# Optimization experiments

Measured on AMD Instinct MI355X. Metric: run time of the kernel, lower is better.

Reference implementation:

```python
import jax, jax.numpy as jnp
import numpy as np
from jax import lax


def setup_inputs() -> dict:
    key = jax.random.key(0)
    k1, k2 = jax.random.split(key)
    L, B, d = 2048, 16, 1024
    x = jax.random.normal(k1, (L, B, d), dtype=jnp.float32)
    val_range = (3.0 / d) ** 0.5
    weight = jax.random.uniform(k2, (d, 3 * d), dtype=jnp.float32,
                                minval=-val_range, maxval=val_range)
    bias = jnp.zeros((2 * d,), dtype=jnp.float32)
    c0 = jnp.zeros((B, d), dtype=jnp.float32)
    return {"x": x, "weight": weight, "bias": bias, "c0": c0}


def reference(x, weight, bias, c0):
    # x: [L, B, d]; weight: [d, 3d]; bias: [2d]; c0: [B, d]
    L, B, d = x.shape
    u = (x.reshape(-1, d) @ weight).reshape(L, B, d, 3)
    x_tilde = u[..., 0]                               # [L, B, d]
    forget = jax.nn.sigmoid(u[..., 1] + bias[:d])     # [L, B, d]
    reset = jax.nn.sigmoid(u[..., 2] + bias[d:])      # [L, B, d]
    # k == 3 case: x_prime is the raw input (highway connection)
    x_prime = x

    def step(c_prev, ft_xt):
        ft, xt = ft_xt
        c = (c_prev - xt) * ft + xt
        return c, c

    c_last, cs = lax.scan(step, c0, (forget, x_tilde))
    g = jnp.tanh(cs)  # activation_type == 1
    h = (g - x_prime) * reset + x_prime
    return h, c_last
```

## Files before the change

kernel.cpp:

```cpp
#include <hip/hip_runtime.h>

#define L_SEQ 2048
#define BATCH 16
#define DDIM  1024
#define MDIM  (L_SEQ * BATCH)
#define NDIM  (3 * DDIM)
#define KDIM  DDIM
#define CH    (BATCH * DDIM)
#define NSEG  32
#define SEGL  64

typedef __attribute__((ext_vector_type(8))) short short8;
typedef __attribute__((ext_vector_type(4))) float f32x4;

static __device__ __forceinline__ unsigned short f2bf(float f) {
  unsigned int u = __builtin_bit_cast(unsigned int, f);
  unsigned int lsb = (u >> 16) & 1u;
  u += 0x7fffu + lsb;
  return (unsigned short)(u >> 16);
}
static __device__ __forceinline__ float bf2f(unsigned short s) {
  unsigned int u = ((unsigned int)s) << 16;
  return __builtin_bit_cast(float, u);
}

static __device__ __forceinline__ void gll16(const void* g, void* l) {
  __builtin_amdgcn_global_load_lds(
      (const __attribute__((address_space(1))) unsigned int*)g,
      (__attribute__((address_space(3))) unsigned int*)l, 16, 0, 0);
}


__global__ void k_convert_x(const float4* __restrict__ x, ushort4* __restrict__ xb, int n4) {
  int i = blockIdx.x * blockDim.x + threadIdx.x;
  int stride = gridDim.x * blockDim.x;
  for (; i < n4; i += stride) {
    float4 v = x[i];
    ushort4 o;
    o.x = f2bf(v.x); o.y = f2bf(v.y); o.z = f2bf(v.z); o.w = f2bf(v.w);
    xb[i] = o;
  }
}

__global__ void k_convert_w(const float* __restrict__ w, unsigned short* __restrict__ wb) {
  int gid = blockIdx.x * 256 + threadIdx.x;
  int k = gid & (KDIM - 1);
  int n = gid >> 10;
  int col = (n < DDIM) ? 3 * n : (n < 2 * DDIM) ? 3 * (n - DDIM) + 1 : 3 * (n - 2 * DDIM) + 2;
  wb[gid] = f2bf(w[(size_t)k * NDIM + col]);
}


#define MFMA1(I, J, A, B) \
  acc[I][J] = __builtin_amdgcn_mfma_f32_16x16x32_bf16(A, B, acc[I][J], 0, 0, 0);

#define MFMAQ(BASE, A0, A1, A2, A3, B0, B1, B2, B3)      \
  MFMA1(BASE + 0, 0, A0, B0) MFMA1(BASE + 0, 1, A0, B1)  \
  MFMA1(BASE + 0, 2, A0, B2) MFMA1(BASE + 0, 3, A0, B3)  \
  MFMA1(BASE + 1, 0, A1, B0) MFMA1(BASE + 1, 1, A1, B1)  \
  MFMA1(BASE + 1, 2, A1, B2) MFMA1(BASE + 1, 3, A1, B3)  \
  MFMA1(BASE + 2, 0, A2, B0) MFMA1(BASE + 2, 1, A2, B1)  \
  MFMA1(BASE + 2, 2, A2, B2) MFMA1(BASE + 2, 3, A2, B3)  \
  MFMA1(BASE + 3, 0, A3, B0) MFMA1(BASE + 3, 1, A3, B1)  \
  MFMA1(BASE + 3, 2, A3, B2) MFMA1(BASE + 3, 3, A3, B3)

#define TILE64(T) do {                                                        \
  const char* bufC = LDSc + ((T) & 1) * 65536;                                \
  char*       bufN = LDSc + (((T) + 1) & 1) * 65536;                          \
  const int stA = (((T) + 1) & 15) * 128;                                     \
         \
  gll16(srcA0 + stA, bufN + dstOff);                                          \
  gll16(srcA1 + stA, bufN + 8192 + dstOff);                                   \
  gll16(srcB0 + stA, bufN + 32768 + dstOff);                                  \
  gll16(srcB1 + stA, bufN + 40960 + dstOff);                                  \
  gll16(srcA0 + stA + 64, bufN + 16384 + dstOff);                             \
  gll16(srcA1 + stA + 64, bufN + 24576 + dstOff);                             \
  gll16(srcB0 + stA + 64, bufN + 49152 + dstOff);                             \
  gll16(srcB1 + stA + 64, bufN + 57344 + dstOff);                             \
  __builtin_amdgcn_sched_barrier(0);                                          \
      \
  a0 = *(const short8*)(bufC + aRd);                                          \
  a1 = *(const short8*)(bufC + aRd + 1024);                                   \
  a2 = *(const short8*)(bufC + aRd + 2048);                                   \
  a3 = *(const short8*)(bufC + aRd + 3072);                                   \
  b0 = *(const short8*)(bufC + 32768 + bRd);                                  \
  b1 = *(const short8*)(bufC + 32768 + bRd + 1024);                           \
  b2 = *(const short8*)(bufC + 32768 + bRd + 2048);                           \
  b3 = *(const short8*)(bufC + 32768 + bRd + 3072);                           \
  na0 = *(const short8*)(bufC + aRd + 4096);                                  \
  na1 = *(const short8*)(bufC + aRd + 5120);                                  \
  na2 = *(const short8*)(bufC + aRd + 6144);                                  \
  na3 = *(const short8*)(bufC + aRd + 7168);                                  \
  __builtin_amdgcn_s_setprio(1);                                              \
  MFMAQ(0, a0, a1, a2, a3, b0, b1, b2, b3)                                    \
  __builtin_amdgcn_s_setprio(0);                                              \
  a0 = *(const short8*)(bufC + 16384 + aRd);                                  \
  a1 = *(const short8*)(bufC + 16384 + aRd + 1024);                           \
  a2 = *(const short8*)(bufC + 16384 + aRd + 2048);                           \
  a3 = *(const short8*)(bufC + 16384 + aRd + 3072);                           \
  nb0 = *(const short8*)(bufC + 49152 + bRd);                                 \
  nb1 = *(const short8*)(bufC + 49152 + bRd + 1024);                          \
  nb2 = *(const short8*)(bufC + 49152 + bRd + 2048);                          \
  nb3 = *(const short8*)(bufC + 49152 + bRd + 3072);                          \
  __builtin_amdgcn_s_setprio(1);                                              \
  MFMAQ(4, na0, na1, na2, na3, b0, b1, b2, b3)                                \
  __builtin_amdgcn_s_setprio(0);                                              \
  na0 = *(const short8*)(bufC + 16384 + aRd + 4096);                          \
  na1 = *(const short8*)(bufC + 16384 + aRd + 5120);                          \
  na2 = *(const short8*)(bufC + 16384 + aRd + 6144);                          \
  na3 = *(const short8*)(bufC + 16384 + aRd + 7168);                          \
  __builtin_amdgcn_s_setprio(1);                                              \
  MFMAQ(0, a0, a1, a2, a3, nb0, nb1, nb2, nb3)                                \
  MFMAQ(4, na0, na1, na2, na3, nb0, nb1, nb2, nb3)                            \
  __builtin_amdgcn_s_setprio(0);                                              \
          \
  asm volatile("s_waitcnt vmcnt(0)" ::: "memory");                            \
  __builtin_amdgcn_s_barrier();                                               \
} while (0)

__global__ __launch_bounds__(512, 2) void k_gemm256(
    const unsigned short* __restrict__ xb,
    const unsigned short* __restrict__ wb,
    const float* __restrict__ bias,
    unsigned short* __restrict__ xtb,
    unsigned short* __restrict__ fbuf,
    unsigned short* __restrict__ rbuf) {
  __shared__ char LDS[131072];
  char* LDSc = LDS;

  const int tid  = threadIdx.x;
  const int lane = tid & 63;
  const int wid  = tid >> 6;
  const int wr   = wid >> 2;
  const int wc   = wid & 3;

  int bid = blockIdx.x;
  int wg = (bid & 7) * 192 + (bid >> 3);
  int mt = wg / 12;
  int nt = wg - mt * 12;
  const int rowBase = mt * 256;
  const int colBase = nt * 256;

  const int l15 = lane & 15;
  const int sl  = lane >> 4;
  const int ra0 = wr * 128 + l15;
  const int rb0 = wc * 64 + l15;
  const int aRd = ra0 * 64 + (sl ^ ((ra0 >> 1) & 3)) * 16;
  const int bRd = rb0 * 64 + (sl ^ ((rb0 >> 1) & 3)) * 16;

  const int p0i = tid, p1i = 512 + tid;
  const int r0 = p0i >> 2, r1 = p1i >> 2;
  const int s0 = (p0i & 3) ^ ((r0 >> 1) & 3);
  const int s1 = (p1i & 3) ^ ((r1 >> 1) & 3);
  const char* srcA0 = (const char*)xb + (size_t)(rowBase + r0) * 2048 + s0 * 16;
  const char* srcA1 = (const char*)xb + (size_t)(rowBase + r1) * 2048 + s1 * 16;
  const char* srcB0 = (const char*)wb + (size_t)(colBase + r0) * 2048 + s0 * 16;
  const char* srcB1 = (const char*)wb + (size_t)(colBase + r1) * 2048 + s1 * 16;
  const int dstOff = wid * 1024;

  f32x4 acc[8][4];
#pragma unroll
  for (int ii = 0; ii < 8; ++ii)
#pragma unroll
    for (int jj = 0; jj < 4; ++jj)
      acc[ii][jj] = (f32x4){0.f, 0.f, 0.f, 0.f};

  gll16(srcA0, LDSc + dstOff);
  gll16(srcA1, LDSc + 8192 + dstOff);
  gll16(srcB0, LDSc + 32768 + dstOff);
  gll16(srcB1, LDSc + 40960 + dstOff);
  gll16(srcA0 + 64, LDSc + 16384 + dstOff);
  gll16(srcA1 + 64, LDSc + 24576 + dstOff);
  gll16(srcB0 + 64, LDSc + 49152 + dstOff);
  gll16(srcB1 + 64, LDSc + 57344 + dstOff);
  asm volatile("s_waitcnt vmcnt(0)" ::: "memory");
  __builtin_amdgcn_s_barrier();

  short8 a0, a1, a2, a3, na0, na1, na2, na3;
  short8 b0, b1, b2, b3, nb0, nb1, nb2, nb3;

  for (int i = 0; i < 8; ++i) {
    TILE64(2 * i);
    TILE64(2 * i + 1);
  }

  const int region = colBase >> 10;
#pragma unroll
  for (int qm = 0; qm < 2; ++qm) {
#pragma unroll
    for (int m = 0; m < 4; ++m) {
      int grow = rowBase + wr * 128 + qm * 64 + m * 16 + ((lane >> 4) << 2);
#pragma unroll
      for (int n = 0; n < 4; ++n) {
        int gcol = colBase + wc * 64 + n * 16 + (lane & 15);
        f32x4 v = acc[qm * 4 + m][n];
        if (region == 0) {
#pragma unroll
          for (int j = 0; j < 4; ++j)
            xtb[(size_t)(grow + j) * DDIM + gcol] = f2bf(v[j]);
        } else {
          float bv = bias[gcol - DDIM];
          unsigned short* dst = (region == 1) ? fbuf : rbuf;
          int lcol = gcol - (region << 10);
#pragma unroll
          for (int j = 0; j < 4; ++j) {
            float sg = 1.0f / (1.0f + __expf(-(v[j] + bv)));
            dst[(size_t)(grow + j) * DDIM + lcol] = f2bf(sg);
          }
        }
      }
    }
  }
}


__global__ __launch_bounds__(256) void k_scan1(
    const unsigned short* __restrict__ fbuf,
    const unsigned short* __restrict__ xtb,
    float4* __restrict__ AB) {
  int chp = blockIdx.x * 256 + threadIdx.x;
  int seg = blockIdx.y;
  size_t base = (size_t)seg * SEGL * CH + chp * 2;
  const unsigned int* fp = (const unsigned int*)(fbuf + base);
  const unsigned int* xp = (const unsigned int*)(xtb + base);
  float a0 = 1.f, a1 = 1.f, b0 = 0.f, b1 = 0.f;
#pragma unroll 8
  for (int s = 0; s < SEGL; ++s) {
    unsigned int fv = fp[(size_t)s * (CH / 2)];
    unsigned int xv = xp[(size_t)s * (CH / 2)];
    float f0 = bf2f((unsigned short)fv), f1 = bf2f((unsigned short)(fv >> 16));
    float x0 = bf2f((unsigned short)xv), x1 = bf2f((unsigned short)(xv >> 16));
    b0 = (b0 - x0) * f0 + x0;  a0 *= f0;
    b1 = (b1 - x1) * f1 + x1;  a1 *= f1;
  }
  AB[(size_t)seg * (CH / 2) + chp] = (float4){a0, b0, a1, b1};
}


__global__ __launch_bounds__(256) void k_scan2(
    const float* __restrict__ c0,
    const float4* __restrict__ AB,
    float* __restrict__ Cin,
    float* __restrict__ clast) {
  int chp = blockIdx.x * 256 + threadIdx.x;
  float2 cc = ((const float2*)c0)[chp];
  float ca = cc.x, cb = cc.y;
#pragma unroll
  for (int s = 0; s < NSEG; ++s) {
    ((float2*)Cin)[(size_t)s * (CH / 2) + chp] = (float2){ca, cb};
    float4 ab = AB[(size_t)s * (CH / 2) + chp];
    ca = ca * ab.x + ab.y;
    cb = cb * ab.z + ab.w;
  }
  ((float2*)clast)[chp] = (float2){ca, cb};
}


__global__ __launch_bounds__(256) void k_scan3(
    const float* __restrict__ x,
    const unsigned short* __restrict__ fbuf,
    const unsigned short* __restrict__ xtb,
    const unsigned short* __restrict__ rbuf,
    const float* __restrict__ Cin,
    float* __restrict__ h) {
  int chp = blockIdx.x * 256 + threadIdx.x;
  int seg = blockIdx.y;
  float2 cc = ((const float2*)Cin)[(size_t)seg * (CH / 2) + chp];
  float ca = cc.x, cb = cc.y;
  size_t base = (size_t)seg * SEGL * CH + chp * 2;
  const unsigned int* fp = (const unsigned int*)(fbuf + base);
  const unsigned int* tp = (const unsigned int*)(xtb + base);
  const unsigned int* rp = (const unsigned int*)(rbuf + base);
  const float2* xp = (const float2*)(x + base);
  float2* hp = (float2*)(h + base);
#pragma unroll 4
  for (int s = 0; s < SEGL; ++s) {
    unsigned int fv = fp[(size_t)s * (CH / 2)];
    unsigned int tv = tp[(size_t)s * (CH / 2)];
    unsigned int rv = rp[(size_t)s * (CH / 2)];
    float2 xv = xp[(size_t)s * (CH / 2)];
    float f0 = bf2f((unsigned short)fv), f1 = bf2f((unsigned short)(fv >> 16));
    float t0 = bf2f((unsigned short)tv), t1 = bf2f((unsigned short)(tv >> 16));
    float r0 = bf2f((unsigned short)rv), r1 = bf2f((unsigned short)(rv >> 16));
    ca = (ca - t0) * f0 + t0;
    cb = (cb - t1) * f1 + t1;
    float e0 = __expf(-2.f * fabsf(ca));
    float e1 = __expf(-2.f * fabsf(cb));
    float g0 = copysignf((1.f - e0) / (1.f + e0), ca);
    float g1 = copysignf((1.f - e1) / (1.f + e1), cb);
    float h0 = (g0 - xv.x) * r0 + xv.x;
    float h1 = (g1 - xv.y) * r1 + xv.y;
    hp[(size_t)s * (CH / 2)] = (float2){h0, h1};
  }
}


extern "C" void kernel_launch(void* const* d_in, const int* in_sizes, int n_in,
                              void* d_out, int out_size, void* d_ws, size_t ws_size,
                              hipStream_t stream) {
  const float* x    = (const float*)d_in[0];
  const float* w    = (const float*)d_in[1];
  const float* bias = (const float*)d_in[2];
  const float* c0   = (const float*)d_in[3];
  float* out = (float*)d_out;
  char* ws = (char*)d_ws;

  unsigned short* wb   = (unsigned short*)(ws);
  float4*         AB   = (float4*)(ws);
  float*          Cin  = (float*)(ws + 4194304);
  unsigned short* xtb  = (unsigned short*)(ws + 6291456);
  unsigned short* fbuf = (unsigned short*)(ws + 73400320);
  unsigned short* rbuf = (unsigned short*)(ws + 140509184);
  unsigned short* xb = (unsigned short*)d_out;

  k_convert_x<<<2048, 256, 0, stream>>>((const float4*)x, (ushort4*)xb, MDIM * KDIM / 4);
  k_convert_w<<<(NDIM * KDIM) / 256, 256, 0, stream>>>(w, wb);

  k_gemm256<<<1536, 512, 0, stream>>>(xb, wb, bias, xtb, fbuf, rbuf);

  k_scan1<<<dim3(32, NSEG), 256, 0, stream>>>(fbuf, xtb, AB);
  k_scan2<<<32, 256, 0, stream>>>(c0, AB, Cin, out + (size_t)L_SEQ * CH);
  k_scan3<<<dim3(32, NSEG), 256, 0, stream>>>(x, fbuf, xtb, rbuf, Cin, out);
}
```

Before: 426.2 us.

## Shrink GEMM macro-tile from 256x256 to 128x128 with 4-wave blocks

Replaces the 256x256, 512-thread GEMM tile (with a 64-wide K step and a 128KB double-buffered LDS) by a 128x128 tile using 256 threads and a 32-wide K step. It uses 32KB of LDS and targets 3 blocks per CU. The aim is higher occupancy and more blocks to hide latency. In exchange, each tile does less arithmetic per byte loaded, so global and LDS traffic per FLOP doubles. It also drops the setprio and interleaved-load scheduling, and issues one barrier per 32-wide K step.

Measured after the change: 463.1 us. 1.09x slower.

```diff
diff --git a/kernel.cpp b/kernel.cpp
--- a/kernel.cpp
+++ b/kernel.cpp
@@ -54,101 +54,62 @@
 #define MFMA1(I, J, A, B) \
   acc[I][J] = __builtin_amdgcn_mfma_f32_16x16x32_bf16(A, B, acc[I][J], 0, 0, 0);
 
-#define MFMAQ(BASE, A0, A1, A2, A3, B0, B1, B2, B3)      \
-  MFMA1(BASE + 0, 0, A0, B0) MFMA1(BASE + 0, 1, A0, B1)  \
-  MFMA1(BASE + 0, 2, A0, B2) MFMA1(BASE + 0, 3, A0, B3)  \
-  MFMA1(BASE + 1, 0, A1, B0) MFMA1(BASE + 1, 1, A1, B1)  \
-  MFMA1(BASE + 1, 2, A1, B2) MFMA1(BASE + 1, 3, A1, B3)  \
-  MFMA1(BASE + 2, 0, A2, B0) MFMA1(BASE + 2, 1, A2, B1)  \
-  MFMA1(BASE + 2, 2, A2, B2) MFMA1(BASE + 2, 3, A2, B3)  \
-  MFMA1(BASE + 3, 0, A3, B0) MFMA1(BASE + 3, 1, A3, B1)  \
-  MFMA1(BASE + 3, 2, A3, B2) MFMA1(BASE + 3, 3, A3, B3)
-
-#define TILE64(T) do {                                                        \
-  const char* bufC = LDSc + ((T) & 1) * 65536;                                \
-  char*       bufN = LDSc + (((T) + 1) & 1) * 65536;                          \
-  const int stA = (((T) + 1) & 15) * 128;                                     \
-         \
-  gll16(srcA0 + stA, bufN + dstOff);                                          \
-  gll16(srcA1 + stA, bufN + 8192 + dstOff);                                   \
-  gll16(srcB0 + stA, bufN + 32768 + dstOff);                                  \
-  gll16(srcB1 + stA, bufN + 40960 + dstOff);                                  \
-  gll16(srcA0 + stA + 64, bufN + 16384 + dstOff);                             \
-  gll16(srcA1 + stA + 64, bufN + 24576 + dstOff);                             \
-  gll16(srcB0 + stA + 64, bufN + 49152 + dstOff);                             \
-  gll16(srcB1 + stA + 64, bufN + 57344 + dstOff);                             \
+#define TILE32(T) do {                                                        \
+  const char* bufC = LDSc + ((T) & 1) * 16384;                                \
+  char*       bufN = LDSc + (((T) + 1) & 1) * 16384;                          \
+  const int kb = (((T) + 1) & 31) * 64;                                       \
+  gll16(srcA0 + kb, bufN + dstOff);                                           \
+  gll16(srcA1 + kb, bufN + 4096 + dstOff);                                    \
+  gll16(srcB0 + kb, bufN + 8192 + dstOff);                                    \
+  gll16(srcB1 + kb, bufN + 12288 + dstOff);                                   \
   __builtin_amdgcn_sched_barrier(0);                                          \
-      \
   a0 = *(const short8*)(bufC + aRd);                                          \
   a1 = *(const short8*)(bufC + aRd + 1024);                                   \
   a2 = *(const short8*)(bufC + aRd + 2048);                                   \
   a3 = *(const short8*)(bufC + aRd + 3072);                                   \
-  b0 = *(const short8*)(bufC + 32768 + bRd);                                  \
-  b1 = *(const short8*)(bufC + 32768 + bRd + 1024);                           \
-  b2 = *(const short8*)(bufC + 32768 + bRd + 2048);                           \
-  b3 = *(const short8*)(bufC + 32768 + bRd + 3072);                           \
-  na0 = *(const short8*)(bufC + aRd + 4096);                                  \
-  na1 = *(const short8*)(bufC + aRd + 5120);                                  \
-  na2 = *(const short8*)(bufC + aRd + 6144);                                  \
-  na3 = *(const short8*)(bufC + aRd + 7168);                                  \
-  __builtin_amdgcn_s_setprio(1);                                              \
-  MFMAQ(0, a0, a1, a2, a3, b0, b1, b2, b3)                                    \
-  __builtin_amdgcn_s_setprio(0);                                              \
-  a0 = *(const short8*)(bufC + 16384 + aRd);                                  \
-  a1 = *(const short8*)(bufC + 16384 + aRd + 1024);                           \
-  a2 = *(const short8*)(bufC + 16384 + aRd + 2048);                           \
-  a3 = *(const short8*)(bufC + 16384 + aRd + 3072);                           \
-  nb0 = *(const short8*)(bufC + 49152 + bRd);                                 \
-  nb1 = *(const short8*)(bufC + 49152 + bRd + 1024);                          \
-  nb2 = *(const short8*)(bufC + 49152 + bRd + 2048);                          \
-  nb3 = *(const short8*)(bufC + 49152 + bRd + 3072);                          \
-  __builtin_amdgcn_s_setprio(1);                                              \
-  MFMAQ(4, na0, na1, na2, na3, b0, b1, b2, b3)                                \
-  __builtin_amdgcn_s_setprio(0);                                              \
-  na0 = *(const short8*)(bufC + 16384 + aRd + 4096);                          \
-  na1 = *(const short8*)(bufC + 16384 + aRd + 5120);                          \
-  na2 = *(const short8*)(bufC + 16384 + aRd + 6144);                          \
-  na3 = *(const short8*)(bufC + 16384 + aRd + 7168);                          \
-  __builtin_amdgcn_s_setprio(1);                                              \
-  MFMAQ(0, a0, a1, a2, a3, nb0, nb1, nb2, nb3)                                \
-  MFMAQ(4, na0, na1, na2, na3, nb0, nb1, nb2, nb3)                            \
-  __builtin_amdgcn_s_setprio(0);                                              \
-          \
+  b0 = *(const short8*)(bufC + 8192 + bRd);                                   \
+  b1 = *(const short8*)(bufC + 8192 + bRd + 1024);                            \
+  b2 = *(const short8*)(bufC + 8192 + bRd + 2048);                            \
+  b3 = *(const short8*)(bufC + 8192 + bRd + 3072);                            \
+  MFMA1(0, 0, a0, b0) MFMA1(0, 1, a0, b1) MFMA1(0, 2, a0, b2) MFMA1(0, 3, a0, b3) \
+  MFMA1(1, 0, a1, b0) MFMA1(1, 1, a1, b1) MFMA1(1, 2, a1, b2) MFMA1(1, 3, a1, b3) \
+  MFMA1(2, 0, a2, b0) MFMA1(2, 1, a2, b1) MFMA1(2, 2, a2, b2) MFMA1(2, 3, a2, b3) \
+  MFMA1(3, 0, a3, b0) MFMA1(3, 1, a3, b1) MFMA1(3, 2, a3, b2) MFMA1(3, 3, a3, b3) \
   asm volatile("s_waitcnt vmcnt(0)" ::: "memory");                            \
   __builtin_amdgcn_s_barrier();                                               \
 } while (0)
 
-__global__ __launch_bounds__(512, 2) void k_gemm256(
+__global__ __launch_bounds__(256, 3) void k_gemm128(
     const unsigned short* __restrict__ xb,
     const unsigned short* __restrict__ wb,
     const float* __restrict__ bias,
     unsigned short* __restrict__ xtb,
     unsigned short* __restrict__ fbuf,
     unsigned short* __restrict__ rbuf) {
-  __shared__ char LDS[131072];
+  __shared__ char LDS[32768];
   char* LDSc = LDS;
 
   const int tid  = threadIdx.x;
   const int lane = tid & 63;
   const int wid  = tid >> 6;
-  const int wr   = wid >> 2;
-  const int wc   = wid & 3;
+  const int wr   = wid >> 1;
+  const int wc   = wid & 1;
 
   int bid = blockIdx.x;
-  int wg = (bid & 7) * 192 + (bid >> 3);
-  int mt = wg / 12;
-  int nt = wg - mt * 12;
-  const int rowBase = mt * 256;
-  const int colBase = nt * 256;
+  int wg = (bid & 7) * 768 + (bid >> 3);
+  int mt = wg / 24;
+  int nt = wg - mt * 24;
+  const int rowBase = mt * 128;
+  const int colBase = nt * 128;
 
   const int l15 = lane & 15;
   const int sl  = lane >> 4;
-  const int ra0 = wr * 128 + l15;
+  const int ra0 = wr * 64 + l15;
   const int rb0 = wc * 64 + l15;
   const int aRd = ra0 * 64 + (sl ^ ((ra0 >> 1) & 3)) * 16;
   const int bRd = rb0 * 64 + (sl ^ ((rb0 >> 1) & 3)) * 16;
 
-  const int p0i = tid, p1i = 512 + tid;
+  const int p0i = tid, p1i = 256 + tid;
   const int r0 = p0i >> 2, r1 = p1i >> 2;
   const int s0 = (p0i & 3) ^ ((r0 >> 1) & 3);
   const int s1 = (p1i & 3) ^ ((r1 >> 1) & 3);
@@ -158,55 +119,48 @@
   const char* srcB1 = (const char*)wb + (size_t)(colBase + r1) * 2048 + s1 * 16;
   const int dstOff = wid * 1024;
 
-  f32x4 acc[8][4];
-#pragma unroll
-  for (int ii = 0; ii < 8; ++ii)
+  f32x4 acc[4][4];
+#pragma unroll
+  for (int ii = 0; ii < 4; ++ii)
 #pragma unroll
     for (int jj = 0; jj < 4; ++jj)
       acc[ii][jj] = (f32x4){0.f, 0.f, 0.f, 0.f};
 
   gll16(srcA0, LDSc + dstOff);
-  gll16(srcA1, LDSc + 8192 + dstOff);
-  gll16(srcB0, LDSc + 32768 + dstOff);
-  gll16(srcB1, LDSc + 40960 + dstOff);
-  gll16(srcA0 + 64, LDSc + 16384 + dstOff);
-  gll16(srcA1 + 64, LDSc + 24576 + dstOff);
-  gll16(srcB0 + 64, LDSc + 49152 + dstOff);
-  gll16(srcB1 + 64, LDSc + 57344 + dstOff);
+  gll16(srcA1, LDSc + 4096 + dstOff);
+  gll16(srcB0, LDSc + 8192 + dstOff);
+  gll16(srcB1, LDSc + 12288 + dstOff);
   asm volatile("s_waitcnt vmcnt(0)" ::: "memory");
   __builtin_amdgcn_s_barrier();
 
-  short8 a0, a1, a2, a3, na0, na1, na2, na3;
-  short8 b0, b1, b2, b3, nb0, nb1, nb2, nb3;
-
-  for (int i = 0; i < 8; ++i) {
-    TILE64(2 * i);
-    TILE64(2 * i + 1);
+  short8 a0, a1, a2, a3;
+  short8 b0, b1, b2, b3;
+
+  for (int i = 0; i < 16; ++i) {
+    TILE32(2 * i);
+    TILE32(2 * i + 1);
   }
 
   const int region = colBase >> 10;
 #pragma unroll
-  for (int qm = 0; qm < 2; ++qm) {
-#pragma unroll
-    for (int m = 0; m < 4; ++m) {
-      int grow = rowBase + wr * 128 + qm * 64 + m * 16 + ((lane >> 4) << 2);
-#pragma unroll
-      for (int n = 0; n < 4; ++n) {
-        int gcol = colBase + wc * 64 + n * 16 + (lane & 15);
-        f32x4 v = acc[qm * 4 + m][n];
-        if (region == 0) {
-#pragma unroll
-          for (int j = 0; j < 4; ++j)
-            xtb[(size_t)(grow + j) * DDIM + gcol] = f2bf(v[j]);
-        } else {
-          float bv = bias[gcol - DDIM];
-          unsigned short* dst = (region == 1) ? fbuf : rbuf;
-          int lcol = gcol - (region << 10);
-#pragma unroll
-          for (int j = 0; j < 4; ++j) {
-            float sg = 1.0f / (1.0f + __expf(-(v[j] + bv)));
-            dst[(size_t)(grow + j) * DDIM + lcol] = f2bf(sg);
-          }
+  for (int m = 0; m < 4; ++m) {
+    int grow = rowBase + wr * 64 + m * 16 + ((lane >> 4) << 2);
+#pragma unroll
+    for (int n = 0; n < 4; ++n) {
+      int gcol = colBase + wc * 64 + n * 16 + (lane & 15);
+      f32x4 v = acc[m][n];
+      if (region == 0) {
+#pragma unroll
+        for (int j = 0; j < 4; ++j)
+          xtb[(size_t)(grow + j) * DDIM + gcol] = f2bf(v[j]);
+      } else {
+        float bv = bias[gcol - DDIM];
+        unsigned short* dst = (region == 1) ? fbuf : rbuf;
+        int lcol = gcol - (region << 10);
+#pragma unroll
+        for (int j = 0; j < 4; ++j) {
+          float sg = 1.0f / (1.0f + __expf(-(v[j] + bv)));
+          dst[(size_t)(grow + j) * DDIM + lcol] = f2bf(sg);
         }
       }
     }
@@ -316,7 +270,7 @@
   k_convert_x<<<2048, 256, 0, stream>>>((const float4*)x, (ushort4*)xb, MDIM * KDIM / 4);
   k_convert_w<<<(NDIM * KDIM) / 256, 256, 0, stream>>>(w, wb);
 
-  k_gemm256<<<1536, 512, 0, stream>>>(xb, wb, bias, xtb, fbuf, rbuf);
+  k_gemm128<<<6144, 256, 0, stream>>>(xb, wb, bias, xtb, fbuf, rbuf);
 
   k_scan1<<<dim3(32, NSEG), 256, 0, stream>>>(fbuf, xtb, AB);
   k_scan2<<<32, 256, 0, stream>>>(c0, AB, Cin, out + (size_t)L_SEQ * CH);
```
